# Kernel tuning notes

Measured on AMD Instinct MI355X. Metric: run time of the kernel, lower is better.

## Reference

```python
import jax, jax.numpy as jnp
import numpy as np


def setup_inputs() -> dict:
    key = jax.random.key(0)
    k1, k2 = jax.random.split(key)
    B, S, D, K = 16, 4096, 256, 4096
    x = jax.random.normal(k1, (B, S, D), dtype=jnp.float32)
    scale = 1.0 / K  # matches nn.init.uniform_(-scale, scale)
    embeddings = jax.random.uniform(k2, (K, D), dtype=jnp.float32, minval=-scale, maxval=scale)
    return {"x": x, "embeddings": embeddings}


def reference(x, embeddings):
    # Flatten all leading dims: [N, D]
    in_shape = x.shape
    flat = x.reshape(-1, in_shape[-1])
    distances = (
        jnp.sum(flat ** 2, axis=1, keepdims=True)
        + jnp.sum(embeddings ** 2, axis=1)
        - 2.0 * flat @ embeddings.T
    )
    proposal = jnp.argmin(distances, axis=-1).reshape(in_shape[:-1])  # [B, S] int
    quantized = embeddings[proposal]  # [B, S, D] gather
    return quantized, proposal
```

## Files before the change

kernel.cpp:

```cpp
#include <hip/hip_runtime.h>
#include <hip/hip_bf16.h>
#include <stdint.h>

#define NROWS 65536
#define DDIM  256
#define KCAND 4096
#define CAP   48
#define MARGIN1 8e-4f
#define MARGIN2 8e-4f

#define LSTRIDE 132
#define ROWS_PB 128

typedef __bf16 bf16x8 __attribute__((ext_vector_type(8)));
typedef float  f32x4  __attribute__((ext_vector_type(4)));
typedef unsigned int u32;
typedef unsigned long long u64;

__device__ __forceinline__ u32 f2bf_u(float f) {
    u32 u = __float_as_uint(f);
    u += 0x7fffu + ((u >> 16) & 1u);
    return u >> 16;
}
__device__ __forceinline__ u32 pack2(float lo, float hi) { return f2bf_u(lo) | (f2bf_u(hi) << 16); }
__device__ __forceinline__ u32 fkey(float f) {
    u32 u = __float_as_uint(f);
    return (u & 0x80000000u) ? ~u : (u | 0x80000000u);
}
__device__ __forceinline__ float funkey(u32 k) {
    u32 u = (k & 0x80000000u) ? (k ^ 0x80000000u) : ~k;
    return __uint_as_float(u);
}
__device__ __forceinline__ float vmax4(f32x4 v) {
    return fmaxf(fmaxf(v[0], v[1]), fmaxf(v[2], v[3]));
}

__device__ __forceinline__ float exact_r4(const float* __restrict__ xr, float A,
                                          const float* __restrict__ er) {
    float b = 0.f, acc = 0.f;
    #pragma unroll 8
    for (int q = 0; q < DDIM / 4; ++q) {
        float4 e  = ((const float4*)er)[q];
        float4 xv = ((const float4*)xr)[q];
        b = fmaf(e.x, e.x, b);  acc = fmaf(2.0f * xv.x, e.x, acc);
        b = fmaf(e.y, e.y, b);  acc = fmaf(2.0f * xv.y, e.y, acc);
        b = fmaf(e.z, e.z, b);  acc = fmaf(2.0f * xv.z, e.z, acc);
        b = fmaf(e.w, e.w, b);  acc = fmaf(2.0f * xv.w, e.w, acc);
    }
    return (A + b) - acc;
}

__launch_bounds__(256)
__global__ void convert_e(const float* __restrict__ e, u32* __restrict__ ebf) {
    int T = blockIdx.x * blockDim.x + threadIdx.x;
    int L = T & 63, u = (T >> 6) & 3, kc = (T >> 8) & 7, s = T >> 11;
    int cand = s * 64 + u * 16 + (L & 15);
    int k0 = kc * 32 + (L >> 4) * 8;
    const float4* src = (const float4*)(e + (size_t)cand * DDIM + k0);
    float4 a = src[0], b = src[1];
    uint4 o;
    o.x = pack2(a.x, a.y); o.y = pack2(a.z, a.w);
    o.z = pack2(b.x, b.y); o.w = pack2(b.z, b.w);
    ((uint4*)ebf)[T] = o;
}

__launch_bounds__(256, 2)
__global__ void phase1(const float* __restrict__ x, const u32* __restrict__ ebf,
                       u32* __restrict__ cnt, uint2* __restrict__ list) {
    __shared__ u32 lxd[ROWS_PB * LSTRIDE];
    __shared__ u32 rowBestK[ROWS_PB];

    const int tid = threadIdx.x;
    const int rowBase = blockIdx.x * ROWS_PB;
    if (tid < ROWS_PB) rowBestK[tid] = 0x007FFFFFu;

    {
        const float4* x4 = (const float4*)(x + (size_t)rowBase * DDIM);
        #pragma unroll
        for (int j = 0; j < 32; ++j) {
            int idx = j * 256 + tid;
            int r = idx >> 6, c4 = idx & 63;
            float4 v = x4[idx];
            *(uint2*)&lxd[r * LSTRIDE + 2 * c4] = make_uint2(pack2(v.x, v.y), pack2(v.z, v.w));
        }
    }
    __syncthreads();

    const int L = tid & 63;
    const int w = __builtin_amdgcn_readfirstlane(tid >> 6);
    const int lq = L >> 4, ln = L & 15;
    const int vL = L << 4;

    const char* ebc_w = (const char*)ebf + (size_t)w * 32768;

    auto loadB = [&](int it_, int kc_, bf16x8* dst) {
        const char* kb = ebc_w + (size_t)it_ * 131072 + kc_ * 4096;
        #pragma unroll
        for (int u = 0; u < 4; ++u)
            dst[u] = *(const bf16x8*)(kb + u * 1024 + vL);
    };

    const char* pa = (const char*)lxd + ln * (LSTRIDE * 4) + lq * 16;

    bf16x8 bb[2][4];
    f32x4 acc[8][4];
    const f32x4 Z4 = {0.f, 0.f, 0.f, 0.f};

    loadB(0, 0, bb[0]);
    #pragma unroll
    for (int kc = 0; kc < 8; ++kc) {
        if (kc < 7) loadB(0, kc + 1, bb[(kc + 1) & 1]);
        #pragma unroll
        for (int a = 0; a < 8; ++a) {
            bf16x8 fa = *(const bf16x8*)(pa + a * (16 * LSTRIDE * 4) + kc * 64);
            #pragma unroll
            for (int u = 0; u < 4; ++u)
                acc[a][u] = (kc == 0)
                    ? __builtin_amdgcn_mfma_f32_16x16x32_bf16(bb[0][u], fa, Z4, 0, 0, 0)
                    : __builtin_amdgcn_mfma_f32_16x16x32_bf16(bb[kc & 1][u], fa, acc[a][u], 0, 0, 0);
        }
    }
    #pragma unroll
    for (int a = 0; a < 8; ++a) {
        float lmax = fmaxf(fmaxf(vmax4(acc[a][0]), vmax4(acc[a][1])),
                           fmaxf(vmax4(acc[a][2]), vmax4(acc[a][3])));
        float m = fmaxf(lmax, __shfl_xor(lmax, 16, 64));
        m = fmaxf(m, __shfl_xor(m, 32, 64));
        if (lq == 0) atomicMax(&rowBestK[a * 16 + ln], fkey(m));
    }
    __syncthreads();

    loadB(0, 0, bb[0]);
    #pragma unroll 1
    for (int it = 0; it < 16; ++it) {
        {
            loadB(it, 1, bb[1]);
            #pragma unroll
            for (int a = 0; a < 8; ++a) {
                bf16x8 fa = *(const bf16x8*)(pa + a * (16 * LSTRIDE * 4));
                #pragma unroll
                for (int u = 0; u < 4; ++u)
                    acc[a][u] = __builtin_amdgcn_mfma_f32_16x16x32_bf16(bb[0][u], fa, Z4, 0, 0, 0);
            }
        }
        #pragma unroll
        for (int kc = 1; kc < 8; ++kc) {
            int g = it * 8 + kc;
            if (g < 127) { int gn = g + 1; loadB(gn >> 3, gn & 7, bb[(kc + 1) & 1]); }
            #pragma unroll
            for (int a = 0; a < 8; ++a) {
                bf16x8 fa = *(const bf16x8*)(pa + a * (16 * LSTRIDE * 4) + kc * 64);
                #pragma unroll
                for (int u = 0; u < 4; ++u)
                    acc[a][u] = __builtin_amdgcn_mfma_f32_16x16x32_bf16(bb[kc & 1][u], fa, acc[a][u], 0, 0, 0);
            }
        }

        int strip = it * 4 + w;
        u32 seen[8];
        #pragma unroll
        for (int a = 0; a < 8; ++a) seen[a] = rowBestK[a * 16 + ln];

        #pragma unroll
        for (int a = 0; a < 8; ++a) {
            float lmax = fmaxf(fmaxf(vmax4(acc[a][0]), vmax4(acc[a][1])),
                               fmaxf(vmax4(acc[a][2]), vmax4(acc[a][3])));
            float m = fmaxf(lmax, __shfl_xor(lmax, 16, 64));
            m = fmaxf(m, __shfl_xor(m, 32, 64));
            if (lq == 0) atomicMax(&rowBestK[a * 16 + ln], fkey(m));
            float eff  = fmaxf(m, funkey(seen[a]));
            float thrA = eff - 0.5f * MARGIN1;
            if (__ballot(lmax >= thrA)) {
                int c = 0;
                #pragma unroll
                for (int u = 0; u < 4; ++u)
                    #pragma unroll
                    for (int r = 0; r < 4; ++r)
                        c += (acc[a][u][r] >= thrA) ? 1 : 0;
                int p = c, t;
                t = __shfl_up(p, 16, 64); if (lq >= 1) p += t;
                t = __shfl_up(p, 32, 64); if (lq >= 2) p += t;
                int grow = rowBase + a * 16 + ln;
                u32 base = 0;
                if (lq == 3 && p > 0) base = atomicAdd(&cnt[grow], (u32)p);
                base = __shfl(base, 48 + ln, 64);
                u32 pos = base + (u32)(p - c);
                #pragma unroll
                for (int u = 0; u < 4; ++u)
                    #pragma unroll
                    for (int r = 0; r < 4; ++r) {
                        float av = acc[a][u][r];
                        if (av >= thrA) {
                            if (pos < CAP)
                                list[(size_t)grow * CAP + pos] =
                                    make_uint2(__float_as_uint(-2.f * av),
                                               (u32)(strip * 64 + u * 16 + lq * 4 + r));
                            ++pos;
                        }
                    }
            }
        }
    }
}

__launch_bounds__(256)
__global__ void phase2(const float* __restrict__ x, const float* __restrict__ emb,
                       const u32* __restrict__ cnt, const uint2* __restrict__ list,
                       float* __restrict__ outq, float* __restrict__ outp) {
    __shared__ float xs[4][DDIM];
    const int wid = threadIdx.x >> 6;
    const int row = blockIdx.x * 4 + wid;
    const int L   = threadIdx.x & 63;

    u32 n = cnt[row];
    u32 kstar;

    if (n == 1) {
        kstar = list[(size_t)row * CAP].y;
    } else {
        bool scan_all = (n > CAP);
        bool resolved = false;
        float vv = INFINITY; u32 kk = 0;
        bool surv = false;
        if (!scan_all) {
            if (L < (int)n) { uint2 e = list[(size_t)row * CAP + L]; vv = __uint_as_float(e.x); kk = e.y; }
            float mv = vv;
            #pragma unroll
            for (int o = 32; o; o >>= 1) mv = fminf(mv, __shfl_xor(mv, o, 64));
            surv = (L < (int)n) && (vv <= mv + MARGIN2);
            u64 bal = __ballot(surv);
            if (__popcll(bal) == 1) {
                kstar = __shfl(kk, (int)(__ffsll(bal) - 1), 64);
                resolved = true;
            }
        }
        if (!resolved) {
            float4 v = ((const float4*)(x + (size_t)row * DDIM))[L];
            *(float4*)&xs[wid][L * 4] = v;
            double s = (double)v.x * v.x + (double)v.y * v.y + (double)v.z * v.z + (double)v.w * v.w;
            #pragma unroll
            for (int o = 32; o; o >>= 1) s += __shfl_xor(s, o, 64);
            float A = (float)s;

            u64 key = 0xFFFFFFFFFFFFFFFFull;
            if (!scan_all) {
                if (surv) {
                    float r = exact_r4(xs[wid], A, emb + (size_t)kk * DDIM);
                    key = ((u64)fkey(r) << 32) | (u64)kk;
                }
            } else {
                for (int c = 0; c < KCAND / 64; ++c) {
                    u32 k = (u32)(c * 64 + L);
                    float r = exact_r4(xs[wid], A, emb + (size_t)k * DDIM);
                    u64 cand = ((u64)fkey(r) << 32) | (u64)k;
                    key = (cand < key) ? cand : key;
                }
            }
            #pragma unroll
            for (int o = 32; o; o >>= 1) {
                u64 other = __shfl_xor(key, o, 64);
                key = (other < key) ? other : key;
            }
            kstar = (u32)(key & 0xFFFFFFFFull);
        }
    }

    float4 q = ((const float4*)(emb + (size_t)kstar * DDIM))[L];
    ((float4*)(outq + (size_t)row * DDIM))[L] = q;
    if (L == 0) outp[row] = (float)kstar;
}

extern "C" void kernel_launch(void* const* d_in, const int* in_sizes, int n_in,
                              void* d_out, int out_size, void* d_ws, size_t ws_size,
                              hipStream_t stream) {
    const float* x   = (const float*)d_in[0];
    const float* emb = (const float*)d_in[1];
    float* outq = (float*)d_out;
    float* outp = outq + (size_t)NROWS * DDIM;

    char* ws = (char*)d_ws;
    u32*   ebf  = (u32*)ws;
    u32*   cnt  = (u32*)(ws + (2u << 20));
    uint2* list = (uint2*)(ws + (3u << 20));

    hipMemsetAsync(cnt, 0, (size_t)NROWS * sizeof(u32), stream);
    convert_e<<<512, 256, 0, stream>>>(emb, ebf);
    phase1<<<NROWS / ROWS_PB, 256, 0, stream>>>(x, ebf, cnt, list);
    phase2<<<NROWS / 4, 256, 0, stream>>>(x, emb, cnt, list, outq, outp);
}
```

Before: 390.3 us.

## Fuse easy-row resolution into phase1 and queue ambiguous rows for rescue

Phase1 now resolves rows with a single clear candidate at the end of its own block and writes the gathered embedding and index directly. Rows it cannot resolve are appended to a global queue through an atomic counter, and a smaller grid-stride rescue kernel handles only those rows. This avoids launching one wave per row for all 65536 rows in a separate phase2 pass. In exchange phase1 gets extra tail work, a block barrier and atomics.

```diff
diff --git a/kernel.cpp b/kernel.cpp
--- a/kernel.cpp
+++ b/kernel.cpp
@@ -66,7 +66,10 @@
 
 __launch_bounds__(256, 2)
 __global__ void phase1(const float* __restrict__ x, const u32* __restrict__ ebf,
-                       u32* __restrict__ cnt, uint2* __restrict__ list) {
+                       const float* __restrict__ emb,
+                       u32* __restrict__ cnt, uint2* __restrict__ list,
+                       u32* __restrict__ qcnt, u32* __restrict__ qids,
+                       float* __restrict__ outq, float* __restrict__ outp) {
     __shared__ u32 lxd[ROWS_PB * LSTRIDE];
     __shared__ u32 rowBestK[ROWS_PB];
 
@@ -201,23 +204,56 @@
             }
         }
     }
+
+    __syncthreads();
+
+    for (int rr = 0; rr < 32; ++rr) {
+        int grow = rowBase + w * 32 + rr;
+        u32 n = cnt[grow];
+        u32 kstar = 0;
+        bool resolved = false;
+        if (n == 1) {
+            kstar = list[(size_t)grow * CAP].y;
+            resolved = true;
+        } else if (n <= CAP) {
+            float vv = INFINITY; u32 kk = 0;
+            if (L < (int)n) { uint2 e = list[(size_t)grow * CAP + L]; vv = __uint_as_float(e.x); kk = e.y; }
+            float mv = vv;
+            #pragma unroll
+            for (int o = 32; o; o >>= 1) mv = fminf(mv, __shfl_xor(mv, o, 64));
+            bool surv = (L < (int)n) && (vv <= mv + MARGIN2);
+            u64 bal = __ballot(surv);
+            if (__popcll(bal) == 1) {
+                kstar = __shfl(kk, (int)(__ffsll(bal) - 1), 64);
+                resolved = true;
+            }
+        }
+        if (resolved) {
+            float4 q = ((const float4*)(emb + (size_t)kstar * DDIM))[L];
+            ((float4*)(outq + (size_t)grow * DDIM))[L] = q;
+            if (L == 0) outp[grow] = (float)kstar;
+        } else {
+            if (L == 0) { u32 qi = atomicAdd(qcnt, 1u); qids[qi] = (u32)grow; }
+        }
+    }
 }
 
 __launch_bounds__(256)
-__global__ void phase2(const float* __restrict__ x, const float* __restrict__ emb,
-                       const u32* __restrict__ cnt, const uint2* __restrict__ list,
-                       float* __restrict__ outq, float* __restrict__ outp) {
+__global__ void rescue2(const float* __restrict__ x, const float* __restrict__ emb,
+                        const u32* __restrict__ cnt, const uint2* __restrict__ list,
+                        const u32* __restrict__ qcnt, const u32* __restrict__ qids,
+                        float* __restrict__ outq, float* __restrict__ outp) {
     __shared__ float xs[4][DDIM];
     const int wid = threadIdx.x >> 6;
-    const int row = blockIdx.x * 4 + wid;
     const int L   = threadIdx.x & 63;
-
-    u32 n = cnt[row];
-    u32 kstar;
-
-    if (n == 1) {
-        kstar = list[(size_t)row * CAP].y;
-    } else {
+    const int wave0 = blockIdx.x * 4 + wid;
+    const u32 nq = *qcnt;
+
+    for (u32 qi = (u32)wave0; qi < nq; qi += 8192) {
+        const int row = (int)qids[qi];
+        const u32 n = cnt[row];
+        u32 kstar;
+
         bool scan_all = (n > CAP);
         bool resolved = false;
         float vv = INFINITY; u32 kk = 0;
@@ -263,11 +299,11 @@
             }
             kstar = (u32)(key & 0xFFFFFFFFull);
         }
-    }
-
-    float4 q = ((const float4*)(emb + (size_t)kstar * DDIM))[L];
-    ((float4*)(outq + (size_t)row * DDIM))[L] = q;
-    if (L == 0) outp[row] = (float)kstar;
+
+        float4 q = ((const float4*)(emb + (size_t)kstar * DDIM))[L];
+        ((float4*)(outq + (size_t)row * DDIM))[L] = q;
+        if (L == 0) outp[row] = (float)kstar;
+    }
 }
 
 extern "C" void kernel_launch(void* const* d_in, const int* in_sizes, int n_in,
@@ -281,10 +317,12 @@
     char* ws = (char*)d_ws;
     u32*   ebf  = (u32*)ws;
     u32*   cnt  = (u32*)(ws + (2u << 20));
+    u32*   qcnt = (u32*)(ws + (2u << 20) + (256u << 10));
+    u32*   qids = (u32*)(ws + (2u << 20) + (256u << 10) + 64);
     uint2* list = (uint2*)(ws + (3u << 20));
 
-    hipMemsetAsync(cnt, 0, (size_t)NROWS * sizeof(u32), stream);
+    hipMemsetAsync(cnt, 0, (size_t)(256u << 10) + 64, stream);
     convert_e<<<512, 256, 0, stream>>>(emb, ebf);
-    phase1<<<NROWS / ROWS_PB, 256, 0, stream>>>(x, ebf, cnt, list);
-    phase2<<<NROWS / 4, 256, 0, stream>>>(x, emb, cnt, list, outq, outp);
-}
+    phase1<<<NROWS / ROWS_PB, 256, 0, stream>>>(x, ebf, emb, cnt, list, qcnt, qids, outq, outp);
+    rescue2<<<2048, 256, 0, stream>>>(x, emb, cnt, list, qcnt, qids, outq, outp);
+}
```

New measurement: 779.9 us. 2x slower.
